# Kernel tuning notes

Hardware: AMD Instinct MI355X
Metric: run time of the kernel (lower is better)

## Reference

```python
import jax, jax.numpy as jnp
import numpy as np

N = 8192
N_DIM = 7
N_WIDTH = 64


def setup_inputs() -> dict:
    key = jax.random.key(0)
    ks = jax.random.split(key, 12)
    scale = 0.05
    u = lambda k, shape: scale * (2.0 * jax.random.uniform(k, shape) - 1.0)
    # Linear params stored as (in, out) so forward uses x @ W + b (same math as torch Linear).
    lin = lambda k, fan_in, fan_out: (
        jax.random.uniform(jax.random.fold_in(k, 0), (fan_in, fan_out),
                           minval=-1.0, maxval=1.0) / np.sqrt(fan_in),
        jax.random.uniform(jax.random.fold_in(k, 1), (fan_out,),
                           minval=-1.0, maxval=1.0) / np.sqrt(fan_in),
    )
    W1, b1 = lin(ks[1], N_DIM, N_WIDTH)
    W2, b2 = lin(ks[2], N_WIDTH, N_WIDTH)
    Wl, bl = lin(ks[3], N_WIDTH, 1)
    return {
        "x": jax.random.normal(ks[0], (N, N_DIM), dtype=jnp.float32),
        "alpha": jax.random.uniform(ks[4], (1,)),          # Edges.alpha = 1 * rand(1)
        "W1": W1, "b1": b1, "wt1": u(ks[5], (N_WIDTH, N_WIDTH)), "bs1": u(ks[6], (1,)),
        "W2": W2, "b2": b2, "wt2": u(ks[7], (N_WIDTH, N_WIDTH)), "bs2": u(ks[8], (1,)),
        "Wl": Wl, "bl": bl,
    }


def _edges(x, alpha):
    eta, phi = x[:, 1], x[:, 2]
    deta = eta[:, None] - eta[None, :]                      # (n, n)
    dphi = jnp.abs(phi[:, None] - phi[None, :])
    dphi = jnp.where(dphi > jnp.pi, 2.0 * jnp.pi - dphi, dphi)
    dRdR = deta * deta + dphi * dphi
    A = jnp.exp(-alpha[0] * dRdR)
    return jax.nn.softmax(A, axis=1) + jnp.eye(x.shape[0], dtype=x.dtype)


def _gcn_layer(X, A, W, b, wt, bs):
    X = jax.nn.relu(X @ W + b)                              # embed + relu
    X = (A @ X) @ wt + bs[0]                                # aggregate + mix + scalar bias
    return jax.nn.relu(X)


def reference(x, alpha, W1, b1, wt1, bs1, W2, b2, wt2, bs2, Wl, bl):
    A = _edges(x, alpha)
    V = jax.nn.relu(_gcn_layer(x, A, W1, b1, wt1, bs1))
    V = jax.nn.relu(_gcn_layer(V, A, W2, b2, wt2, bs2))
    s = V.sum(axis=0)                                       # (n_width,)
    return jax.nn.sigmoid(s @ Wl + bl)                      # (1,)
```

## Files before the change

### kernel.cpp

```cpp
#include <hip/hip_runtime.h>
#include <math.h>

#define NN 8192
#define L2E 1.44269504088896340736f
#define TWO_PI 6.28318530717958647693f

typedef _Float16 h8 __attribute__((ext_vector_type(8)));
typedef _Float16 h4 __attribute__((ext_vector_type(4)));
typedef float f32x4 __attribute__((ext_vector_type(4)));
typedef float f32x2 __attribute__((ext_vector_type(2)));
#define MFMA16(A, B, C) __builtin_amdgcn_mfma_f32_16x16x32_f16(A, B, C, 0, 0, 0)

#define GLD_LDS16(gsrc, ldst)                                          \
  __builtin_amdgcn_global_load_lds(                                    \
      (const __attribute__((address_space(1))) unsigned int*)(gsrc),   \
      (__attribute__((address_space(3))) unsigned int*)(ldst), 16, 0, 0)

union V8 { float4 v[2]; float f[8]; };

__global__ __launch_bounds__(256) void prep_kernel(
    const float* __restrict__ x, const float* __restrict__ alpha,
    const float* __restrict__ W1, const float* __restrict__ b1,
    float* __restrict__ eta_s, float* __restrict__ phi_s,
    float* __restrict__ H1, _Float16* __restrict__ HT1,
    float* __restrict__ svec)
{
  __shared__ float sW[448];
  __shared__ float sb[64];
  __shared__ float T[32][68];
  const int t = threadIdx.x;
  if (blockIdx.x == 0 && t < 64) svec[t] = 0.f;
  for (int k = t; k < 448; k += 256) sW[k] = W1[k];
  if (t < 64) sb[t] = b1[t];
  const float s = sqrtf(alpha[0] * L2E);
  const int i0 = blockIdx.x * 32;
  const int r = t >> 3, q = t & 7;
  const int i = i0 + r;
  float xv[7];
#pragma unroll
  for (int k = 0; k < 7; k++) xv[k] = x[i * 7 + k];
  if (q == 0) { eta_s[i] = xv[1] * s; phi_s[i] = xv[2] * s; }
  __syncthreads();
#pragma unroll
  for (int c = 0; c < 8; c++) {
    const int n = q * 8 + c;
    float hv = sb[n];
#pragma unroll
    for (int k = 0; k < 7; k++) hv = fmaf(xv[k], sW[k * 64 + n], hv);
    T[r][n] = fmaxf(hv, 0.f);
  }
  __syncthreads();
  for (int e = t; e < 512; e += 256)
    *(f32x4*)(H1 + (size_t)i0 * 64 + (e << 2)) =
        *(const f32x4*)&T[e >> 4][(e << 2) & 63];
  const int n = t >> 2, sg = (t & 3) * 8;
  h8 v;
#pragma unroll
  for (int ss = 0; ss < 8; ss++) v[ss] = (_Float16)T[sg + ss][n];
  *(h8*)(HT1 + (size_t)n * NN + i0 + sg) = v;
}

template <bool NEED_L>
__global__ __launch_bounds__(256, 4) void attn_pass(
    const float* __restrict__ eta_s, const float* __restrict__ phi_s,
    const _Float16* __restrict__ HT, const float* __restrict__ alpha,
    float* __restrict__ Ypart, float* __restrict__ lpart)
{
  __shared__ __align__(16) char smem[32768];
  _Float16* stage = (_Float16*)smem;
  const int tid = threadIdx.x;
  const int w = tid >> 6, lane = tid & 63, m = lane & 15, g = lane >> 4;
  const int tile = blockIdx.x >> 2, part = blockIdx.x & 3;
  const int i0 = tile << 5;
  const int jbase = part << 11;
  const float Cs = TWO_PI * sqrtf(alpha[0] * L2E);
  const float et0 = eta_s[i0 + m],      ph0 = phi_s[i0 + m];
  const float et1 = eta_s[i0 + 16 + m], ph1 = phi_s[i0 + 16 + m];

  const int r0 = tid >> 4, gq = tid & 15;
  const _Float16* sbase = HT + (size_t)r0 * NN + ((gq ^ r0) << 3) + jbase;

  f32x4 a00 = {0,0,0,0}, a01 = {0,0,0,0}, a02 = {0,0,0,0}, a03 = {0,0,0,0};
  f32x4 a10 = {0,0,0,0}, a11 = {0,0,0,0}, a12 = {0,0,0,0}, a13 = {0,0,0,0};
  f32x4 l0a = {0,0,0,0}, l1a = {0,0,0,0};
  const h8 onesv = {(_Float16)1.f, (_Float16)1.f, (_Float16)1.f, (_Float16)1.f,
                    (_Float16)1.f, (_Float16)1.f, (_Float16)1.f, (_Float16)1.f};

  const float* ep = eta_s + jbase + (w << 5) + (g << 3);
  const float* pp = phi_s + jbase + (w << 5) + (g << 3);
  V8 E0, P0, E1, P1;
  E0.v[0] = *(const float4*)ep;  E0.v[1] = *(const float4*)(ep + 4);
  P0.v[0] = *(const float4*)pp;  P0.v[1] = *(const float4*)(pp + 4);

#pragma unroll
  for (int k = 0; k < 4; ++k)
    GLD_LDS16(sbase + (size_t)k * 16 * NN, stage + ((k * 256 + tid) << 3));
  __syncthreads();

  const int fs = ((m << 4) + (((w << 2) | g) ^ m)) << 3;

  union AF { h8 v; decltype(__builtin_amdgcn_cvt_pkrtz(0.f, 0.f)) p[4]; };

  auto stage_compute = [&](const V8& Ec, const V8& Pc, const _Float16* cur) {
    const h8 b0 = *(const h8*)(cur + fs);
    const h8 b1 = *(const h8*)(cur + 2048 + fs);
    const h8 b2 = *(const h8*)(cur + 4096 + fs);
    const h8 b3 = *(const h8*)(cur + 6144 + fs);
    AF af0, af1;
#pragma unroll
    for (int tt = 0; tt < 8; tt += 2) {
      const f32x2 pj = {Pc.f[tt], Pc.f[tt + 1]};
      const f32x2 ej = {Ec.f[tt], Ec.f[tt + 1]};
      const f32x2 dp0 = ph0 - pj, dp1 = ph1 - pj;
      const f32x2 ad0 = {fabsf(dp0.x), fabsf(dp0.y)};
      const f32x2 ad1 = {fabsf(dp1.x), fabsf(dp1.y)};
      const f32x2 cm0 = Cs - ad0, cm1 = Cs - ad1;
      const f32x2 wr0 = {fminf(ad0.x, cm0.x), fminf(ad0.y, cm0.y)};
      const f32x2 wr1 = {fminf(ad1.x, cm1.x), fminf(ad1.y, cm1.y)};
      const f32x2 de0 = et0 - ej, de1 = et1 - ej;
      const f32x2 r20 = de0 * de0 + wr0 * wr0;
      const f32x2 r21 = de1 * de1 + wr1 * wr1;
      const f32x2 ax0 = {__builtin_amdgcn_exp2f(-r20.x),
                         __builtin_amdgcn_exp2f(-r20.y)};
      const f32x2 ax1 = {__builtin_amdgcn_exp2f(-r21.x),
                         __builtin_amdgcn_exp2f(-r21.y)};
      const f32x2 ga0 = ax0 * L2E - L2E;
      const f32x2 ga1 = ax1 * L2E - L2E;
      af0.p[tt >> 1] = __builtin_amdgcn_cvt_pkrtz(
          __builtin_amdgcn_exp2f(ga0.x), __builtin_amdgcn_exp2f(ga0.y));
      af1.p[tt >> 1] = __builtin_amdgcn_cvt_pkrtz(
          __builtin_amdgcn_exp2f(ga1.x), __builtin_amdgcn_exp2f(ga1.y));
    }
    a00 = MFMA16(af0.v, b0, a00); a01 = MFMA16(af0.v, b1, a01);
    a02 = MFMA16(af0.v, b2, a02); a03 = MFMA16(af0.v, b3, a03);
    a10 = MFMA16(af1.v, b0, a10); a11 = MFMA16(af1.v, b1, a11);
    a12 = MFMA16(af1.v, b2, a12); a13 = MFMA16(af1.v, b3, a13);
    if constexpr (NEED_L) {
      l0a = MFMA16(af0.v, onesv, l0a);
      l1a = MFMA16(af1.v, onesv, l1a);
    }
  };

#pragma unroll
  for (int s2 = 0; s2 < 8; ++s2) {
    {
      const _Float16* src = sbase + (2 * s2 + 1) * 128;
#pragma unroll
      for (int k = 0; k < 4; ++k)
        GLD_LDS16(src + (size_t)k * 16 * NN,
                  stage + 8192 + ((k * 256 + tid) << 3));
      E1.v[0] = *(const float4*)(ep + s2 * 256 + 128);
      E1.v[1] = *(const float4*)(ep + s2 * 256 + 132);
      P1.v[0] = *(const float4*)(pp + s2 * 256 + 128);
      P1.v[1] = *(const float4*)(pp + s2 * 256 + 132);
      stage_compute(E0, P0, stage);
      __syncthreads();
    }
    {
      if (s2 < 7) {
        const _Float16* src = sbase + (2 * s2 + 2) * 128;
#pragma unroll
        for (int k = 0; k < 4; ++k)
          GLD_LDS16(src + (size_t)k * 16 * NN,
                    stage + ((k * 256 + tid) << 3));
        E0.v[0] = *(const float4*)(ep + s2 * 256 + 256);
        E0.v[1] = *(const float4*)(ep + s2 * 256 + 260);
        P0.v[0] = *(const float4*)(pp + s2 * 256 + 256);
        P0.v[1] = *(const float4*)(pp + s2 * 256 + 260);
      }
      stage_compute(E1, P1, stage + 8192);
      __syncthreads();
    }
  }

  typedef float Red2[32][66];
  Red2* red = (Red2*)smem;
  const int h = w >> 1;
  if ((w & 1) == 0) {
#pragma unroll
    for (int r = 0; r < 4; ++r) {
      red[h][g * 4 + r][m]      = a00[r]; red[h][g * 4 + r][16 + m] = a01[r];
      red[h][g * 4 + r][32 + m] = a02[r]; red[h][g * 4 + r][48 + m] = a03[r];
      red[h][16 + g * 4 + r][m]      = a10[r]; red[h][16 + g * 4 + r][16 + m] = a11[r];
      red[h][16 + g * 4 + r][32 + m] = a12[r]; red[h][16 + g * 4 + r][48 + m] = a13[r];
    }
    if constexpr (NEED_L) {
      if (m == 0) {
#pragma unroll
        for (int r = 0; r < 4; ++r) {
          red[h][g * 4 + r][64]      = l0a[r];
          red[h][16 + g * 4 + r][64] = l1a[r];
        }
      }
    }
  }
  __syncthreads();
  if (w & 1) {
#pragma unroll
    for (int r = 0; r < 4; ++r) {
      red[h][g * 4 + r][m]      += a00[r]; red[h][g * 4 + r][16 + m] += a01[r];
      red[h][g * 4 + r][32 + m] += a02[r]; red[h][g * 4 + r][48 + m] += a03[r];
      red[h][16 + g * 4 + r][m]      += a10[r]; red[h][16 + g * 4 + r][16 + m] += a11[r];
      red[h][16 + g * 4 + r][32 + m] += a12[r]; red[h][16 + g * 4 + r][48 + m] += a13[r];
    }
    if constexpr (NEED_L) {
      if (m == 0) {
#pragma unroll
        for (int r = 0; r < 4; ++r) {
          red[h][g * 4 + r][64]      += l0a[r];
          red[h][16 + g * 4 + r][64] += l1a[r];
        }
      }
    }
  }
  __syncthreads();
#pragma unroll
  for (int k = 0; k < 8; ++k) {
    const int e = tid + k * 256;
    Ypart[((size_t)part * NN + i0 + (e >> 6)) * 64 + (e & 63)] =
        red[0][e >> 6][e & 63] + red[1][e >> 6][e & 63];
  }
  if constexpr (NEED_L) {
    if (tid < 32)
      lpart[(size_t)part * NN + i0 + tid] = red[0][tid][64] + red[1][tid][64];
  }
}

__global__ __launch_bounds__(256) void mid_kernel(
    const float* __restrict__ Yp, const float* __restrict__ lp,
    const float* __restrict__ H1, const float* __restrict__ wt1,
    const float* __restrict__ bs1, const float* __restrict__ W2,
    const float* __restrict__ b2, float* __restrict__ H2,
    _Float16* __restrict__ HT2)
{
  __shared__ float sA[64][68];
  __shared__ float sB[64][68];
  __shared__ float U[16][68];
  __shared__ float sb2v[64];
  const int t = threadIdx.x;
  for (int e = t; e < 1024; e += 256) {
    const int rr = e >> 4, cc = (e << 2) & 63;
    *(f32x4*)&sA[rr][cc] = *(const f32x4*)(wt1 + (e << 2));
    *(f32x4*)&sB[rr][cc] = *(const f32x4*)(W2 + (e << 2));
  }
  if (t < 64) sb2v[t] = b2[t];
  const float bsv = bs1[0];
  const int i0 = blockIdx.x * 16;
  const int r = t >> 4, q = t & 15;
  const int i = i0 + r;
  float l = 0.f;
#pragma unroll
  for (int p = 0; p < 4; ++p) l += lp[(size_t)p * NN + i];
  const float rl = 1.0f / l;
  f32x4 ya = {0, 0, 0, 0};
#pragma unroll
  for (int p = 0; p < 4; ++p)
    ya += *(const f32x4*)(Yp + ((size_t)p * NN + i) * 64 + q * 4);
  const f32x4 h1 = *(const f32x4*)(H1 + (size_t)i * 64 + q * 4);
#pragma unroll
  for (int c = 0; c < 4; ++c) U[r][q * 4 + c] = fmaf(ya[c], rl, h1[c]);
  __syncthreads();
  float z[4];
#pragma unroll
  for (int c = 0; c < 4; ++c) z[c] = bsv;
#pragma unroll
  for (int k4 = 0; k4 < 64; k4 += 4) {
    const f32x4 u4 = *(const f32x4*)&U[r][k4];
#pragma unroll
    for (int kk = 0; kk < 4; ++kk) {
      const f32x4 sa = *(const f32x4*)&sA[k4 + kk][q * 4];
#pragma unroll
      for (int c = 0; c < 4; ++c) z[c] = fmaf(u4[kk], sa[c], z[c]);
    }
  }
  __syncthreads();
#pragma unroll
  for (int c = 0; c < 4; ++c) U[r][q * 4 + c] = fmaxf(z[c], 0.f);
  __syncthreads();
  float hv[4];
#pragma unroll
  for (int c = 0; c < 4; ++c) hv[c] = sb2v[q * 4 + c];
#pragma unroll
  for (int k4 = 0; k4 < 64; k4 += 4) {
    const f32x4 u4 = *(const f32x4*)&U[r][k4];
#pragma unroll
    for (int kk = 0; kk < 4; ++kk) {
      const f32x4 sb4 = *(const f32x4*)&sB[k4 + kk][q * 4];
#pragma unroll
      for (int c = 0; c < 4; ++c) hv[c] = fmaf(u4[kk], sb4[c], hv[c]);
    }
  }
  __syncthreads();
#pragma unroll
  for (int c = 0; c < 4; ++c) U[r][q * 4 + c] = fmaxf(hv[c], 0.f);
  __syncthreads();
  *(f32x4*)(H2 + (size_t)i0 * 64 + (t << 2)) =
      *(const f32x4*)&U[t >> 4][(t << 2) & 63];
  const int n = t >> 2, sg = (t & 3) * 4;
  h4 v;
#pragma unroll
  for (int ss = 0; ss < 4; ss++) v[ss] = (_Float16)U[sg + ss][n];
  *(h4*)(HT2 + (size_t)n * NN + i0 + sg) = v;
}

__global__ __launch_bounds__(256) void final_kernel(
    const float* __restrict__ Yp, const float* __restrict__ lp,
    const float* __restrict__ H2, const float* __restrict__ wt2,
    const float* __restrict__ bs2, float* __restrict__ svec)
{
  __shared__ float sA[64][68];
  __shared__ float U[16][68];
  __shared__ float cred[4][64];
  const int t = threadIdx.x;
  for (int e = t; e < 1024; e += 256) {
    const int rr = e >> 4, cc = (e << 2) & 63;
    *(f32x4*)&sA[rr][cc] = *(const f32x4*)(wt2 + (e << 2));
  }
  const float bsv = bs2[0];
  const int i0 = blockIdx.x * 16;
  const int r = t >> 4, q = t & 15;
  const int i = i0 + r;
  float l = 0.f;
#pragma unroll
  for (int p = 0; p < 4; ++p) l += lp[(size_t)p * NN + i];
  const float rl = 1.0f / l;
  f32x4 ya = {0, 0, 0, 0};
#pragma unroll
  for (int p = 0; p < 4; ++p)
    ya += *(const f32x4*)(Yp + ((size_t)p * NN + i) * 64 + q * 4);
  const f32x4 h2 = *(const f32x4*)(H2 + (size_t)i * 64 + q * 4);
#pragma unroll
  for (int c = 0; c < 4; ++c) U[r][q * 4 + c] = fmaf(ya[c], rl, h2[c]);
  __syncthreads();
  float z[4];
#pragma unroll
  for (int c = 0; c < 4; ++c) z[c] = bsv;
#pragma unroll
  for (int k4 = 0; k4 < 64; k4 += 4) {
    const f32x4 u4 = *(const f32x4*)&U[r][k4];
#pragma unroll
    for (int kk = 0; kk < 4; ++kk) {
      const f32x4 sa = *(const f32x4*)&sA[k4 + kk][q * 4];
#pragma unroll
      for (int c = 0; c < 4; ++c) z[c] = fmaf(u4[kk], sa[c], z[c]);
    }
  }
  __syncthreads();
#pragma unroll
  for (int c = 0; c < 4; ++c) U[r][q * 4 + c] = fmaxf(z[c], 0.f);
  __syncthreads();
  const int col = t & 63, rg = t >> 6;
  float ps = 0.f;
#pragma unroll
  for (int rr = 0; rr < 4; rr++) ps += U[rg * 4 + rr][col];
  cred[rg][col] = ps;
  __syncthreads();
  if (t < 64)
    atomicAdd(svec + t, cred[0][t] + cred[1][t] + cred[2][t] + cred[3][t]);
}

__global__ void out_kernel(const float* __restrict__ svec,
                           const float* __restrict__ Wl,
                           const float* __restrict__ bl,
                           float* __restrict__ out)
{
  const int t = threadIdx.x;
  float v = svec[t] * Wl[t];
#pragma unroll
  for (int off = 32; off > 0; off >>= 1) v += __shfl_down(v, off);
  if (t == 0) {
    const float logit = v + bl[0];
    out[0] = 1.0f / (1.0f + __builtin_amdgcn_exp2f(-logit * L2E));
  }
}

extern "C" void kernel_launch(void* const* d_in, const int* in_sizes, int n_in,
                              void* d_out, int out_size, void* d_ws,
                              size_t ws_size, hipStream_t stream)
{
  const float* x     = (const float*)d_in[0];
  const float* alpha = (const float*)d_in[1];
  const float* W1    = (const float*)d_in[2];
  const float* b1    = (const float*)d_in[3];
  const float* wt1   = (const float*)d_in[4];
  const float* bs1   = (const float*)d_in[5];
  const float* W2    = (const float*)d_in[6];
  const float* b2    = (const float*)d_in[7];
  const float* wt2   = (const float*)d_in[8];
  const float* bs2   = (const float*)d_in[9];
  const float* Wl    = (const float*)d_in[10];
  const float* bl    = (const float*)d_in[11];
  float* out = (float*)d_out;

  char* ws = (char*)d_ws;
  size_t off = 0;
  auto alloc = [&](size_t bytes) {
    void* p = ws + off;
    off = (off + bytes + 255) & ~(size_t)255;
    return p;
  };
  float* eta_s = (float*)alloc(NN * 4 + 256);
  float* phi_s = (float*)alloc(NN * 4 + 256);
  float* H1    = (float*)alloc((size_t)NN * 64 * 4);
  float* H2    = (float*)alloc((size_t)NN * 64 * 4);
  float* Ypart = (float*)alloc((size_t)4 * NN * 64 * 4);
  float* lpart = (float*)alloc((size_t)4 * NN * 4);
  _Float16* HT = (_Float16*)alloc((size_t)NN * 64 * 2 + 512);
  float* svec  = (float*)alloc(64 * 4);

  prep_kernel<<<256, 256, 0, stream>>>(x, alpha, W1, b1, eta_s, phi_s, H1, HT, svec);
  attn_pass<true><<<1024, 256, 0, stream>>>(eta_s, phi_s, HT, alpha, Ypart, lpart);
  mid_kernel<<<512, 256, 0, stream>>>(Ypart, lpart, H1, wt1, bs1, W2, b2, H2, HT);
  attn_pass<false><<<1024, 256, 0, stream>>>(eta_s, phi_s, HT, alpha, Ypart, nullptr);
  final_kernel<<<512, 256, 0, stream>>>(Ypart, lpart, H2, wt2, bs2, svec);
  out_kernel<<<1, 64, 0, stream>>>(svec, Wl, bl, out);
}
```

Baseline: 168.3 us.

## Load HT B-fragments directly from global instead of LDS double-buffer staging

Replaces the double-buffered global_load_lds staging of the HT tile, with its per-stage barriers, by direct per-lane global vector loads of the MFMA B operands inside a fully unrolled loop. This removes the LDS round trip and the __syncthreads between stages, and it shrinks shared memory to just the reduction buffer, which may allow more resident blocks. The cost is that each wave now loads its own B data from global or L2 with strided row accesses, and there is no explicit prefetch to overlap that latency; the compiler has to schedule the loads early enough to hide it.

```diff
diff --git a/kernel.cpp b/kernel.cpp
--- a/kernel.cpp
+++ b/kernel.cpp
@@ -10,11 +10,6 @@
 typedef float f32x4 __attribute__((ext_vector_type(4)));
 typedef float f32x2 __attribute__((ext_vector_type(2)));
 #define MFMA16(A, B, C) __builtin_amdgcn_mfma_f32_16x16x32_f16(A, B, C, 0, 0, 0)
-
-#define GLD_LDS16(gsrc, ldst)                                          \
-  __builtin_amdgcn_global_load_lds(                                    \
-      (const __attribute__((address_space(1))) unsigned int*)(gsrc),   \
-      (__attribute__((address_space(3))) unsigned int*)(ldst), 16, 0, 0)
 
 union V8 { float4 v[2]; float f[8]; };
 
@@ -66,8 +61,7 @@
     const _Float16* __restrict__ HT, const float* __restrict__ alpha,
     float* __restrict__ Ypart, float* __restrict__ lpart)
 {
-  __shared__ __align__(16) char smem[32768];
-  _Float16* stage = (_Float16*)smem;
+  __shared__ __align__(16) float smem[2 * 32 * 66];
   const int tid = threadIdx.x;
   const int w = tid >> 6, lane = tid & 63, m = lane & 15, g = lane >> 4;
   const int tile = blockIdx.x >> 2, part = blockIdx.x & 3;
@@ -77,8 +71,13 @@
   const float et0 = eta_s[i0 + m],      ph0 = phi_s[i0 + m];
   const float et1 = eta_s[i0 + 16 + m], ph1 = phi_s[i0 + 16 + m];
 
-  const int r0 = tid >> 4, gq = tid & 15;
-  const _Float16* sbase = HT + (size_t)r0 * NN + ((gq ^ r0) << 3) + jbase;
+  const int joff = jbase + (w << 5) + (g << 3);
+  const _Float16* hb0 = HT + (size_t)m * NN + joff;
+  const _Float16* hb1 = hb0 + (size_t)16 * NN;
+  const _Float16* hb2 = hb0 + (size_t)32 * NN;
+  const _Float16* hb3 = hb0 + (size_t)48 * NN;
+  const float* ep = eta_s + joff;
+  const float* pp = phi_s + joff;
 
   f32x4 a00 = {0,0,0,0}, a01 = {0,0,0,0}, a02 = {0,0,0,0}, a03 = {0,0,0,0};
   f32x4 a10 = {0,0,0,0}, a11 = {0,0,0,0}, a12 = {0,0,0,0}, a13 = {0,0,0,0};
@@ -86,31 +85,25 @@
   const h8 onesv = {(_Float16)1.f, (_Float16)1.f, (_Float16)1.f, (_Float16)1.f,
                     (_Float16)1.f, (_Float16)1.f, (_Float16)1.f, (_Float16)1.f};
 
-  const float* ep = eta_s + jbase + (w << 5) + (g << 3);
-  const float* pp = phi_s + jbase + (w << 5) + (g << 3);
-  V8 E0, P0, E1, P1;
-  E0.v[0] = *(const float4*)ep;  E0.v[1] = *(const float4*)(ep + 4);
-  P0.v[0] = *(const float4*)pp;  P0.v[1] = *(const float4*)(pp + 4);
-
-#pragma unroll
-  for (int k = 0; k < 4; ++k)
-    GLD_LDS16(sbase + (size_t)k * 16 * NN, stage + ((k * 256 + tid) << 3));
-  __syncthreads();
-
-  const int fs = ((m << 4) + (((w << 2) | g) ^ m)) << 3;
-
   union AF { h8 v; decltype(__builtin_amdgcn_cvt_pkrtz(0.f, 0.f)) p[4]; };
 
-  auto stage_compute = [&](const V8& Ec, const V8& Pc, const _Float16* cur) {
-    const h8 b0 = *(const h8*)(cur + fs);
-    const h8 b1 = *(const h8*)(cur + 2048 + fs);
-    const h8 b2 = *(const h8*)(cur + 4096 + fs);
-    const h8 b3 = *(const h8*)(cur + 6144 + fs);
+#pragma unroll
+  for (int s = 0; s < 16; ++s) {
+    const h8 b0 = *(const h8*)(hb0 + s * 128);
+    const h8 b1 = *(const h8*)(hb1 + s * 128);
+    const h8 b2 = *(const h8*)(hb2 + s * 128);
+    const h8 b3 = *(const h8*)(hb3 + s * 128);
+    V8 E, P;
+    E.v[0] = *(const float4*)(ep + s * 128);
+    E.v[1] = *(const float4*)(ep + s * 128 + 4);
+    P.v[0] = *(const float4*)(pp + s * 128);
+    P.v[1] = *(const float4*)(pp + s * 128 + 4);
+
     AF af0, af1;
 #pragma unroll
     for (int tt = 0; tt < 8; tt += 2) {
-      const f32x2 pj = {Pc.f[tt], Pc.f[tt + 1]};
-      const f32x2 ej = {Ec.f[tt], Ec.f[tt + 1]};
+      const f32x2 pj = {P.f[tt], P.f[tt + 1]};
+      const f32x2 ej = {E.f[tt], E.f[tt + 1]};
       const f32x2 dp0 = ph0 - pj, dp1 = ph1 - pj;
       const f32x2 ad0 = {fabsf(dp0.x), fabsf(dp0.y)};
       const f32x2 ad1 = {fabsf(dp1.x), fabsf(dp1.y)};
@@ -139,38 +132,6 @@
       l0a = MFMA16(af0.v, onesv, l0a);
       l1a = MFMA16(af1.v, onesv, l1a);
     }
-  };
-
-#pragma unroll
-  for (int s2 = 0; s2 < 8; ++s2) {
-    {
-      const _Float16* src = sbase + (2 * s2 + 1) * 128;
-#pragma unroll
-      for (int k = 0; k < 4; ++k)
-        GLD_LDS16(src + (size_t)k * 16 * NN,
-                  stage + 8192 + ((k * 256 + tid) << 3));
-      E1.v[0] = *(const float4*)(ep + s2 * 256 + 128);
-      E1.v[1] = *(const float4*)(ep + s2 * 256 + 132);
-      P1.v[0] = *(const float4*)(pp + s2 * 256 + 128);
-      P1.v[1] = *(const float4*)(pp + s2 * 256 + 132);
-      stage_compute(E0, P0, stage);
-      __syncthreads();
-    }
-    {
-      if (s2 < 7) {
-        const _Float16* src = sbase + (2 * s2 + 2) * 128;
-#pragma unroll
-        for (int k = 0; k < 4; ++k)
-          GLD_LDS16(src + (size_t)k * 16 * NN,
-                    stage + ((k * 256 + tid) << 3));
-        E0.v[0] = *(const float4*)(ep + s2 * 256 + 256);
-        E0.v[1] = *(const float4*)(ep + s2 * 256 + 260);
-        P0.v[0] = *(const float4*)(pp + s2 * 256 + 256);
-        P0.v[1] = *(const float4*)(pp + s2 * 256 + 260);
-      }
-      stage_compute(E1, P1, stage + 8192);
-      __syncthreads();
-    }
   }
 
   typedef float Red2[32][66];
```

Measured after the change: 187.4 us. 1.11x slower.
